# Performance work log

Hardware: AMD Instinct MI355X
Metric: run time of the kernel (lower is better)

Reference implementation:

```python
import jax, jax.numpy as jnp
import numpy as np

TAU = 2.0
V_TH = 1.0
V_RESET = 0.0
ALPHA = 2.0  # ATan surrogate alpha (spikingjelly default)

@jax.custom_vjp
def spike(x):
    # Heaviside forward, ATan surrogate backward
    return (x >= 0).astype(x.dtype)

def _spike_fwd(x):
    return spike(x), x

def _spike_bwd(x, g):
    pix = (jnp.pi / 2) * ALPHA * x
    return (g * (ALPHA / 2) / (1 + pix * pix),)

spike.defvjp(_spike_fwd, _spike_bwd)

def setup_inputs() -> dict:
    key = jax.random.key(0)
    k1, k2, k3 = jax.random.split(key, 3)
    T, B, I, H = 256, 128, 512, 512
    x = jax.random.normal(k1, (T, B, I), dtype=jnp.float32)
    W = jax.random.normal(k2, (H, I), dtype=jnp.float32) * (1.0 / np.sqrt(I))
    b = jax.random.normal(k3, (H,), dtype=jnp.float32) * 0.01
    return {"x": x, "W": W, "b": b}

def reference(x, W, b):
    # Linear projection over all timesteps at once: (T,B,I) @ (H,I)^T -> (T,B,H)
    h = jnp.einsum('tbi,hi->tbh', x, W) + b

    def step(v, ht):
        # LIFNode, decay_input=False, v_reset=0: charge, fire, hard reset
        v = v - (v - V_RESET) / TAU + ht
        s = spike(v - V_TH)
        s_d = jax.lax.stop_gradient(s)  # detach_reset=True
        v = v * (1.0 - s_d) + V_RESET * s_d
        return v, s

    v0 = jnp.zeros_like(h[0])
    _, spikes = jax.lax.scan(step, v0, h)
    # dropout_p=0 (inference) -> identity; no synapse filter
    return spikes
```

## Files before the change

kernel.cpp:

```cpp
#include <hip/hip_runtime.h>

#define T_STEPS 256
#define B_DIM   128
#define I_DIM   512
#define H_DIM   512
#define M_DIM   (T_STEPS * B_DIM)

#define BM 128
#define BN 128
#define BK 32
#define KTILES (I_DIM / BK)

__global__ __launch_bounds__(256, 4) void gemm_bias_f32(
    const float* __restrict__ A,
    const float* __restrict__ Bw,
    const float* __restrict__ bias,
    float* __restrict__ C)
{
    __shared__ float As[BK * BM];
    __shared__ float Bs[BK * BN];

    const int tid = threadIdx.x;
    const int tx  = tid & 15;
    const int ty  = tid >> 4;
    const int m0  = blockIdx.y * BM;
    const int n0  = blockIdx.x * BN;

    float acc[8][8];
    #pragma unroll
    for (int i = 0; i < 8; i++)
        #pragma unroll
        for (int j = 0; j < 8; j++)
            acc[i][j] = 0.0f;

    const int lrow = tid >> 3;
    const int lk   = (tid & 7) * 4;
    const int q    = tid & 7;

    const float* Aptr = A  + (size_t)(m0 + lrow) * I_DIM + lk;
    const float* Bptr = Bw + (size_t)(n0 + lrow) * I_DIM + lk;

    for (int k0 = 0; k0 < I_DIM; k0 += BK) {
        float4 av[4], bv[4];
        #pragma unroll
        for (int p = 0; p < 4; p++) {
            av[p] = *(const float4*)(Aptr + (size_t)(p * 32) * I_DIM + k0);
            bv[p] = *(const float4*)(Bptr + (size_t)(p * 32) * I_DIM + k0);
        }

        __syncthreads();

        #pragma unroll
        for (int p = 0; p < 4; p++) {
            const int r    = lrow + p * 32;
            const int base = (((r >> 2) ^ q) << 2) | (r & 3);
            As[(lk + 0) * BM + base] = av[p].x;
            As[(lk + 1) * BM + base] = av[p].y;
            As[(lk + 2) * BM + base] = av[p].z;
            As[(lk + 3) * BM + base] = av[p].w;
            Bs[(lk + 0) * BN + base] = bv[p].x;
            Bs[(lk + 1) * BN + base] = bv[p].y;
            Bs[(lk + 2) * BN + base] = bv[p].z;
            Bs[(lk + 3) * BN + base] = bv[p].w;
        }

        __syncthreads();

        const float4* As4 = (const float4*)As;
        const float4* Bs4 = (const float4*)Bs;
        for (int k = 0; k < BK; k++) {
            const int rho = (k >> 2) & 7;
            float4 a0 = As4[k * (BM / 4) + ((ty * 2)     ^ rho)];
            float4 a1 = As4[k * (BM / 4) + ((ty * 2 + 1) ^ rho)];
            float4 b0 = Bs4[k * (BN / 4) + (tx        ^ rho)];
            float4 b1 = Bs4[k * (BN / 4) + ((16 + tx) ^ rho)];
            float a[8] = {a0.x, a0.y, a0.z, a0.w, a1.x, a1.y, a1.z, a1.w};
            float b[8] = {b0.x, b0.y, b0.z, b0.w, b1.x, b1.y, b1.z, b1.w};
            #pragma unroll
            for (int i = 0; i < 8; i++)
                #pragma unroll
                for (int j = 0; j < 8; j++)
                    acc[i][j] = fmaf(a[i], b[j], acc[i][j]);
        }
    }

    float4 bc0 = *(const float4*)(bias + n0 + tx * 4);
    float4 bc1 = *(const float4*)(bias + n0 + 64 + tx * 4);

    #pragma unroll
    for (int i = 0; i < 8; i++) {
        const int m = m0 + ty * 8 + i;
        float4 o0, o1;
        o0.x = acc[i][0] + bc0.x;
        o0.y = acc[i][1] + bc0.y;
        o0.z = acc[i][2] + bc0.z;
        o0.w = acc[i][3] + bc0.w;
        o1.x = acc[i][4] + bc1.x;
        o1.y = acc[i][5] + bc1.y;
        o1.z = acc[i][6] + bc1.z;
        o1.w = acc[i][7] + bc1.w;
        float* cp = C + (size_t)m * H_DIM + n0;
        *(float4*)(cp + tx * 4)      = o0;
        *(float4*)(cp + 64 + tx * 4) = o1;
    }
}

#define NCHUNK 4
#define TCHUNK (T_STEPS / NCHUNK)
#define WARM   32
#define SCAN_U 16

__global__ __launch_bounds__(256) void lif_scan(
    const float* __restrict__ h,
    float* __restrict__ out)
{
    const int n     = B_DIM * H_DIM;
    const int chunk = blockIdx.x & (NCHUNK - 1);
    const int idx   = (blockIdx.x >> 2) * 256 + threadIdx.x;
    const float* hp = h + idx;
    float* op       = out + idx;

    const int t_begin = chunk * TCHUNK;
    const int t_start = (chunk == 0) ? 0 : t_begin - WARM;
    const int nb      = (t_begin + TCHUNK - t_start) >> 4;

    float bufA[SCAN_U], bufB[SCAN_U];
    float sA[SCAN_U], sB[SCAN_U];

    #pragma unroll
    for (int i = 0; i < SCAN_U; i++)
        bufA[i] = hp[(size_t)(t_start + i) * n];

    float v = 0.0f;
    int tb = t_start;
    for (int b = 0; b < nb; b += 2) {
        #pragma unroll
        for (int i = 0; i < SCAN_U; i++)
            bufB[i] = hp[(size_t)(tb + SCAN_U + i) * n];

        #pragma unroll
        for (int i = 0; i < SCAN_U; i++) {
            v = 0.5f * v + bufA[i];
            const bool fire = (v >= 1.0f);
            sA[i] = fire ? 1.0f : 0.0f;
            v     = fire ? 0.0f : v;
        }
        if (tb >= t_begin) {
            #pragma unroll
            for (int i = 0; i < SCAN_U; i++)
                op[(size_t)(tb + i) * n] = sA[i];
        }

        if (b + 2 < nb) {
            #pragma unroll
            for (int i = 0; i < SCAN_U; i++)
                bufA[i] = hp[(size_t)(tb + 2 * SCAN_U + i) * n];
        }

        #pragma unroll
        for (int i = 0; i < SCAN_U; i++) {
            v = 0.5f * v + bufB[i];
            const bool fire = (v >= 1.0f);
            sB[i] = fire ? 1.0f : 0.0f;
            v     = fire ? 0.0f : v;
        }
        if (tb + SCAN_U >= t_begin) {
            #pragma unroll
            for (int i = 0; i < SCAN_U; i++)
                op[(size_t)(tb + SCAN_U + i) * n] = sB[i];
        }

        tb += 2 * SCAN_U;
    }
}

extern "C" void kernel_launch(void* const* d_in, const int* in_sizes, int n_in,
                              void* d_out, int out_size, void* d_ws, size_t ws_size,
                              hipStream_t stream) {
    const float* x = (const float*)d_in[0];
    const float* W = (const float*)d_in[1];
    const float* b = (const float*)d_in[2];
    float* out = (float*)d_out;
    float* h   = (float*)d_ws;

    dim3 grid(H_DIM / BN, M_DIM / BM);
    gemm_bias_f32<<<grid, 256, 0, stream>>>(x, W, b, h);

    lif_scan<<<(B_DIM * H_DIM) / 256 * NCHUNK, 256, 0, stream>>>(h, out);
}
```

Baseline: 338.4 us.

## Restructure GEMM to stage full-width weight tile in LDS, read A directly

```diff
diff --git a/kernel.cpp b/kernel.cpp
--- a/kernel.cpp
+++ b/kernel.cpp
@@ -6,25 +6,28 @@
 #define H_DIM   512
 #define M_DIM   (T_STEPS * B_DIM)
 
-#define BM 128
-#define BN 128
 #define BK 32
 #define KTILES (I_DIM / BK)
 
-__global__ __launch_bounds__(256, 4) void gemm_bias_f32(
+__global__ __launch_bounds__(256, 2) void gemm_bias_f32(
     const float* __restrict__ A,
     const float* __restrict__ Bw,
     const float* __restrict__ bias,
     float* __restrict__ C)
 {
-    __shared__ float As[BK * BM];
-    __shared__ float Bs[BK * BN];
+    __shared__ float Bs[I_DIM * BK];
+    float4* Bs4 = (float4*)Bs;
 
-    const int tid = threadIdx.x;
-    const int tx  = tid & 15;
-    const int ty  = tid >> 4;
-    const int m0  = blockIdx.y * BM;
-    const int n0  = blockIdx.x * BN;
+    const int tid  = threadIdx.x;
+    const int lane = tid & 63;
+    const int w    = tid >> 6;
+    const int rho_r = lane & 7;
+    const int rho_w = (tid >> 3) & 7;
+
+    const float* Aw = A + (size_t)(blockIdx.x * 32 + w * 8) * I_DIM;
+
+    const int n_a = tid;
+    const int n_b = tid + 256;
 
     float acc[8][8];
     #pragma unroll
@@ -33,75 +36,81 @@
         for (int j = 0; j < 8; j++)
             acc[i][j] = 0.0f;
 
-    const int lrow = tid >> 3;
-    const int lk   = (tid & 7) * 4;
-    const int q    = tid & 7;
+    for (int kt = 0; kt < KTILES; kt++) {
+        const int k0 = kt * BK;
 
-    const float* Aptr = A  + (size_t)(m0 + lrow) * I_DIM + lk;
-    const float* Bptr = Bw + (size_t)(n0 + lrow) * I_DIM + lk;
-
-    for (int k0 = 0; k0 < I_DIM; k0 += BK) {
-        float4 av[4], bv[4];
+        float4 wva[8], wvb[8];
         #pragma unroll
-        for (int p = 0; p < 4; p++) {
-            av[p] = *(const float4*)(Aptr + (size_t)(p * 32) * I_DIM + k0);
-            bv[p] = *(const float4*)(Bptr + (size_t)(p * 32) * I_DIM + k0);
-        }
+        for (int b = 0; b < 8; b++)
+            wva[b] = *(const float4*)(Bw + (size_t)n_a * I_DIM + k0 + b * 4);
+        #pragma unroll
+        for (int b = 0; b < 8; b++)
+            wvb[b] = *(const float4*)(Bw + (size_t)n_b * I_DIM + k0 + b * 4);
 
         __syncthreads();
 
         #pragma unroll
-        for (int p = 0; p < 4; p++) {
-            const int r    = lrow + p * 32;
-            const int base = (((r >> 2) ^ q) << 2) | (r & 3);
-            As[(lk + 0) * BM + base] = av[p].x;
-            As[(lk + 1) * BM + base] = av[p].y;
-            As[(lk + 2) * BM + base] = av[p].z;
-            As[(lk + 3) * BM + base] = av[p].w;
-            Bs[(lk + 0) * BN + base] = bv[p].x;
-            Bs[(lk + 1) * BN + base] = bv[p].y;
-            Bs[(lk + 2) * BN + base] = bv[p].z;
-            Bs[(lk + 3) * BN + base] = bv[p].w;
-        }
+        for (int b = 0; b < 8; b++)
+            Bs4[n_a * 8 + (b ^ rho_w)] = wva[b];
+        #pragma unroll
+        for (int b = 0; b < 8; b++)
+            Bs4[n_b * 8 + (b ^ rho_w)] = wvb[b];
 
         __syncthreads();
 
-        const float4* As4 = (const float4*)As;
-        const float4* Bs4 = (const float4*)Bs;
-        for (int k = 0; k < BK; k++) {
-            const int rho = (k >> 2) & 7;
-            float4 a0 = As4[k * (BM / 4) + ((ty * 2)     ^ rho)];
-            float4 a1 = As4[k * (BM / 4) + ((ty * 2 + 1) ^ rho)];
-            float4 b0 = Bs4[k * (BN / 4) + (tx        ^ rho)];
-            float4 b1 = Bs4[k * (BN / 4) + ((16 + tx) ^ rho)];
-            float a[8] = {a0.x, a0.y, a0.z, a0.w, a1.x, a1.y, a1.z, a1.w};
-            float b[8] = {b0.x, b0.y, b0.z, b0.w, b1.x, b1.y, b1.z, b1.w};
+        #pragma unroll 2
+        for (int g = 0; g < 8; g++) {
+            float4 a4[8];
+            #pragma unroll
+            for (int i = 0; i < 8; i++)
+                a4[i] = *(const float4*)(Aw + (size_t)i * I_DIM + k0 + g * 4);
+
+            float4 b4[8];
+            #pragma unroll
+            for (int j = 0; j < 8; j++)
+                b4[j] = Bs4[(lane * 8 + j) * 8 + (g ^ rho_r)];
+
             #pragma unroll
             for (int i = 0; i < 8; i++)
                 #pragma unroll
                 for (int j = 0; j < 8; j++)
-                    acc[i][j] = fmaf(a[i], b[j], acc[i][j]);
+                    acc[i][j] = fmaf(a4[i].x, b4[j].x, acc[i][j]);
+            #pragma unroll
+            for (int i = 0; i < 8; i++)
+                #pragma unroll
+                for (int j = 0; j < 8; j++)
+                    acc[i][j] = fmaf(a4[i].y, b4[j].y, acc[i][j]);
+            #pragma unroll
+            for (int i = 0; i < 8; i++)
+                #pragma unroll
+                for (int j = 0; j < 8; j++)
+                    acc[i][j] = fmaf(a4[i].z, b4[j].z, acc[i][j]);
+            #pragma unroll
+            for (int i = 0; i < 8; i++)
+                #pragma unroll
+                for (int j = 0; j < 8; j++)
+                    acc[i][j] = fmaf(a4[i].w, b4[j].w, acc[i][j]);
         }
     }
 
-    float4 bc0 = *(const float4*)(bias + n0 + tx * 4);
-    float4 bc1 = *(const float4*)(bias + n0 + 64 + tx * 4);
+    float4 bi0 = *(const float4*)(bias + lane * 8);
+    float4 bi1 = *(const float4*)(bias + lane * 8 + 4);
 
+    const int m0 = blockIdx.x * 32 + w * 8;
     #pragma unroll
     for (int i = 0; i < 8; i++) {
-        const int m = m0 + ty * 8 + i;
         float4 o0, o1;
-        o0.x = acc[i][0] + bc0.x;
-        o0.y = acc[i][1] + bc0.y;
-        o0.z = acc[i][2] + bc0.z;
-        o0.w = acc[i][3] + bc0.w;
-        o1.x = acc[i][4] + bc1.x;
-        o1.y = acc[i][5] + bc1.y;
-        o1.z = acc[i][6] + bc1.z;
-        o1.w = acc[i][7] + bc1.w;
-        float* cp = C + (size_t)m * H_DIM + n0;
-        *(float4*)(cp + tx * 4)      = o0;
-        *(float4*)(cp + 64 + tx * 4) = o1;
+        o0.x = acc[i][0] + bi0.x;
+        o0.y = acc[i][1] + bi0.y;
+        o0.z = acc[i][2] + bi0.z;
+        o0.w = acc[i][3] + bi0.w;
+        o1.x = acc[i][4] + bi1.x;
+        o1.y = acc[i][5] + bi1.y;
+        o1.z = acc[i][6] + bi1.z;
+        o1.w = acc[i][7] + bi1.w;
+        float* cp = C + (size_t)(m0 + i) * H_DIM + lane * 8;
+        *(float4*)(cp)     = o0;
+        *(float4*)(cp + 4) = o1;
     }
 }
 
@@ -183,8 +192,7 @@
     float* out = (float*)d_out;
     float* h   = (float*)d_ws;
 
-    dim3 grid(H_DIM / BN, M_DIM / BM);
-    gemm_bias_f32<<<grid, 256, 0, stream>>>(x, W, b, h);
+    gemm_bias_f32<<<M_DIM / 32, 256, 0, stream>>>(x, W, b, h);
 
     lif_scan<<<(B_DIM * H_DIM) / 256 * NCHUNK, 256, 0, stream>>>(h, out);
 }
```

Result: slower. 657.4 us (+94.2%).
